# Kernel optimization log

Hardware: AMD Instinct MI355X
Metric: run time of the kernel (lower is better)

The kernel has to match this reference:

```python
import jax, jax.numpy as jnp
import numpy as np

B, D_IN, D_H, N = 16, 32, 64, 4000
ORDER = 2
C_CAT = D_IN + D_H            # 96 channels into each gate conv
C_EFF = (ORDER + 1) * C_CAT   # 288 after order-K diffusion concat


def setup_inputs() -> dict:
    key = jax.random.key(0)
    ks = jax.random.split(key, 9)
    x = jax.random.normal(ks[0], (B, D_IN, N), dtype=jnp.float32)
    h = jax.random.normal(ks[1], (B, D_H, N), dtype=jnp.float32)
    # uniform adjacency, roughly row-normalized to keep diffusion stable
    adj = jax.random.uniform(ks[2], (N, N), dtype=jnp.float32) / N
    scale = 0.05
    Wf = jax.random.normal(ks[3], (D_H, C_EFF), dtype=jnp.float32) * scale
    Wu = jax.random.normal(ks[4], (D_H, C_EFF), dtype=jnp.float32) * scale
    Wc = jax.random.normal(ks[5], (D_H, C_EFF), dtype=jnp.float32) * scale
    bf = jax.random.normal(ks[6], (D_H,), dtype=jnp.float32) * scale
    bu = jax.random.normal(ks[7], (D_H,), dtype=jnp.float32) * scale
    bc = jax.random.normal(ks[8], (D_H,), dtype=jnp.float32) * scale
    return {"x": x, "h": h, "adj": adj, "Wf": Wf, "bf": bf,
            "Wu": Wu, "bu": bu, "Wc": Wc, "bc": bc}


def _spatial_conv(z, adj, W, b):
    # z: [b, c, n]; order-2 diffusion: concat [z, A z, A^2 z] then 1x1 conv
    z1 = jnp.einsum('mn,bcn->bcm', adj, z)
    z2 = jnp.einsum('mn,bcn->bcm', adj, z1)
    feats = jnp.concatenate([z, z1, z2], axis=1)           # [b, 3c, n]
    return jnp.einsum('oc,bcn->bon', W, feats) + b[None, :, None]


def reference(x, h, adj, Wf, bf, Wu, bu, Wc, bc):
    x_gates = jnp.concatenate([x, h], axis=1)              # [b, d_in+d_h, n]
    r = jax.nn.sigmoid(_spatial_conv(x_gates, adj, Wf, bf))
    u = jax.nn.sigmoid(_spatial_conv(x_gates, adj, Wu, bu))
    x_c = jnp.concatenate([x, r * h], axis=1)
    c = jnp.tanh(_spatial_conv(x_c, adj, Wc, bc))
    return u * h + (1.0 - u) * c
```

## Files before the change

### kernel.cpp

```cpp
#include <hip/hip_runtime.h>
#include <cstdint>


#define NREAL 4000
#define NPAD  4096

typedef unsigned short u16;
typedef __attribute__((ext_vector_type(8))) short short8;
typedef __attribute__((ext_vector_type(4))) float f32x4;
typedef __attribute__((ext_vector_type(4))) unsigned short u16x4;

__device__ __forceinline__ u16 f2bf(float f) {
  unsigned u = __builtin_bit_cast(unsigned, f);
  return (u16)((u + 0x7FFFu + ((u >> 16) & 1u)) >> 16);
}
__device__ __forceinline__ float bf2f(u16 b) {
  unsigned u = ((unsigned)b) << 16;
  return __builtin_bit_cast(float, u);
}

__global__ __launch_bounds__(256) void k_pack_adj(const float* __restrict__ adj,
                                                  u16* __restrict__ out) {
  const int idx = blockIdx.x * 256 + threadIdx.x;
  const int m = idx >> 10;
  const int n0 = (idx & 1023) << 2;
  u16x4 o;
  if (m < NREAL && n0 < NREAL) {
    const float4 v = *reinterpret_cast<const float4*>(&adj[(long)m * NREAL + n0]);
    o.x = f2bf(v.x); o.y = f2bf(v.y); o.z = f2bf(v.z); o.w = f2bf(v.w);
  } else {
    o.x = 0; o.y = 0; o.z = 0; o.w = 0;
  }
  *reinterpret_cast<u16x4*>(&out[(long)m * NPAD + n0]) = o;
}

__global__ __launch_bounds__(256) void k_pack_zg(const float* __restrict__ x,
                                                 const float* __restrict__ h,
                                                 u16* __restrict__ zg) {
  const int idx = blockIdx.x * 256 + threadIdx.x;
  const int row = idx >> 10;
  const int n0 = (idx & 1023) << 2;
  const int b = row / 96, c = row % 96;
  const float* src = (c < 32) ? &x[((long)b * 32 + c) * NREAL]
                              : &h[((long)b * 64 + (c - 32)) * NREAL];
  u16x4 o;
  if (n0 < NREAL) {
    const float4 v = *reinterpret_cast<const float4*>(&src[n0]);
    o.x = f2bf(v.x); o.y = f2bf(v.y); o.z = f2bf(v.z); o.w = f2bf(v.w);
  } else {
    o.x = 0; o.y = 0; o.z = 0; o.w = 0;
  }
  *reinterpret_cast<u16x4*>(&zg[(long)row * NPAD + n0]) = o;
}

__global__ __launch_bounds__(256) void k_pack_w(const float* __restrict__ Wf,
                                                const float* __restrict__ Wu,
                                                const float* __restrict__ Wc,
                                                float* __restrict__ Wgt,
                                                float* __restrict__ Wct) {
  const int idx = blockIdx.x * 256 + threadIdx.x;
  if (idx < 288 * 128) {
    const int c = idx >> 7, o = idx & 127;
    Wgt[idx] = (o < 64) ? Wf[o * 288 + c] : Wu[(o - 64) * 288 + c];
  }
  if (idx < 288 * 64) {
    const int c = idx >> 6, o = idx & 63;
    Wct[idx] = Wc[o * 288 + c];
  }
}

template<bool F32OUT>
__global__ __launch_bounds__(256) void k_gemm_bt(const u16* __restrict__ A,
                                                 const u16* __restrict__ B,
                                                 void* __restrict__ Cout,
                                                 int ktPerChunk, long chunkElems) {
  __shared__ __align__(16) u16 As[128 * 32];
  __shared__ __align__(16) u16 Bs[128 * 32];
  const int tid = threadIdx.x;
  const int wave = tid >> 6;
  const int lane = tid & 63;
  const int bn = blockIdx.x;
  const int bm = blockIdx.y;
  const int ktBegin = blockIdx.z * ktPerChunk;
  const int ktEnd = ktBegin + ktPerChunk;

  const int srow = (wave << 4) + (lane >> 2);
  const int sslot = (lane & 3) << 3;
  const long aRow  = (long)(bm * 128 + srow) * NPAD;
  const long aRow2 = aRow + 64L * NPAD;
  const long bRow  = (long)(bn * 128 + srow) * NPAD;
  const long bRow2 = bRow + 64L * NPAD;
  const int wbase = __builtin_amdgcn_readfirstlane(wave << 9);

  const int wr = (wave >> 1) << 6;
  const int wc = (wave & 1) << 6;
  const int fr = lane & 15;
  const int ks = (lane >> 4) << 3;

  f32x4 acc[4][4] = {};

  for (int kt = ktBegin; kt < ktEnd; ++kt) {
    const long kofs = (long)kt * 32 + sslot;
    __syncthreads();
    __builtin_amdgcn_global_load_lds(
        (const __attribute__((address_space(1))) void*)(A + aRow + kofs),
        (__attribute__((address_space(3))) void*)(&As[wbase]), 16, 0, 0);
    __builtin_amdgcn_global_load_lds(
        (const __attribute__((address_space(1))) void*)(A + aRow2 + kofs),
        (__attribute__((address_space(3))) void*)(&As[wbase + 2048]), 16, 0, 0);
    __builtin_amdgcn_global_load_lds(
        (const __attribute__((address_space(1))) void*)(B + bRow + kofs),
        (__attribute__((address_space(3))) void*)(&Bs[wbase]), 16, 0, 0);
    __builtin_amdgcn_global_load_lds(
        (const __attribute__((address_space(1))) void*)(B + bRow2 + kofs),
        (__attribute__((address_space(3))) void*)(&Bs[wbase + 2048]), 16, 0, 0);
    __syncthreads();

    short8 av[4], bv[4];
#pragma unroll
    for (int i = 0; i < 4; ++i) {
      av[i] = *reinterpret_cast<const short8*>(&As[(wr + (i << 4) + fr) * 32 + ks]);
      bv[i] = *reinterpret_cast<const short8*>(&Bs[(wc + (i << 4) + fr) * 32 + ks]);
    }
#pragma unroll
    for (int i = 0; i < 4; ++i)
#pragma unroll
      for (int j = 0; j < 4; ++j)
        acc[i][j] = __builtin_amdgcn_mfma_f32_16x16x32_bf16(av[i], bv[j], acc[i][j], 0, 0, 0);
  }

  const int rb = bm * 128 + wr + ((lane >> 4) << 2);
  const int cb = bn * 128 + wc + fr;
  if (F32OUT) {
    float* C = (float*)Cout + (long)blockIdx.z * chunkElems;
#pragma unroll
    for (int i = 0; i < 4; ++i)
#pragma unroll
      for (int j = 0; j < 4; ++j)
#pragma unroll
        for (int q = 0; q < 4; ++q)
          C[(long)(rb + (i << 4) + q) * NPAD + cb + (j << 4)] = acc[i][j][q];
  } else {
    u16* C = (u16*)Cout;
#pragma unroll
    for (int i = 0; i < 4; ++i)
#pragma unroll
      for (int j = 0; j < 4; ++j)
#pragma unroll
        for (int q = 0; q < 4; ++q)
          C[(long)(rb + (i << 4) + q) * NPAD + cb + (j << 4)] = f2bf(acc[i][j][q]);
  }
}

template<int NC>
__global__ __launch_bounds__(256) void k_combine(const float* __restrict__ P,
                                                 long chunkElems,
                                                 u16* __restrict__ out) {
  const long i4 = ((long)blockIdx.x * 256 + threadIdx.x) * 4;
  f32x4 s = *reinterpret_cast<const f32x4*>(&P[i4]);
#pragma unroll
  for (int c = 1; c < NC; ++c) {
    const f32x4 v = *reinterpret_cast<const f32x4*>(&P[(long)c * chunkElems + i4]);
    s.x += v.x; s.y += v.y; s.z += v.z; s.w += v.w;
  }
  u16x4 o;
  o.x = f2bf(s.x); o.y = f2bf(s.y); o.z = f2bf(s.z); o.w = f2bf(s.w);
  *reinterpret_cast<u16x4*>(&out[i4]) = o;
}

__global__ __launch_bounds__(512) void k_gates(
    const float* __restrict__ x, const float* __restrict__ h,
    const float* __restrict__ Wgt,
    const float* __restrict__ bfv, const float* __restrict__ buv,
    const u16* __restrict__ Z1, const u16* __restrict__ Z2,
    u16* __restrict__ rh_bf, float* __restrict__ rh_f, float* __restrict__ u_f) {
  const int lane = threadIdx.x & 63;
  const int wq = __builtin_amdgcn_readfirstlane(threadIdx.x >> 6);
  const int b = blockIdx.y;
  const int n0 = blockIdx.x * 128 + (lane << 1);
  if (n0 >= NREAL) return;
  const int ob = wq << 4;
  const float* xb = x + (long)b * 32 * NREAL + n0;
  const float* hb = h + (long)b * 64 * NREAL + n0;
  const u16* z1b = Z1 + (long)b * 96 * NPAD + n0;
  const u16* z2b = Z2 + (long)b * 96 * NPAD + n0;

  float a0[16] = {}, a1[16] = {};
#pragma unroll 4
  for (int c = 0; c < 32; ++c) {
    const float2 f = *reinterpret_cast<const float2*>(&xb[(long)c * NREAL]);
#pragma unroll
    for (int oi = 0; oi < 16; ++oi) {
      const float w = Wgt[c * 128 + ob + oi];
      a0[oi] = fmaf(w, f.x, a0[oi]); a1[oi] = fmaf(w, f.y, a1[oi]);
    }
  }
#pragma unroll 4
  for (int c = 0; c < 64; ++c) {
    const float2 f = *reinterpret_cast<const float2*>(&hb[(long)c * NREAL]);
#pragma unroll
    for (int oi = 0; oi < 16; ++oi) {
      const float w = Wgt[(32 + c) * 128 + ob + oi];
      a0[oi] = fmaf(w, f.x, a0[oi]); a1[oi] = fmaf(w, f.y, a1[oi]);
    }
  }
#pragma unroll 4
  for (int c = 0; c < 96; ++c) {
    const unsigned pv = *reinterpret_cast<const unsigned*>(&z1b[(long)c * NPAD]);
    const float f0 = bf2f((u16)(pv & 0xffff)), f1 = bf2f((u16)(pv >> 16));
#pragma unroll
    for (int oi = 0; oi < 16; ++oi) {
      const float w = Wgt[(96 + c) * 128 + ob + oi];
      a0[oi] = fmaf(w, f0, a0[oi]); a1[oi] = fmaf(w, f1, a1[oi]);
    }
  }
#pragma unroll 4
  for (int c = 0; c < 96; ++c) {
    const unsigned pv = *reinterpret_cast<const unsigned*>(&z2b[(long)c * NPAD]);
    const float f0 = bf2f((u16)(pv & 0xffff)), f1 = bf2f((u16)(pv >> 16));
#pragma unroll
    for (int oi = 0; oi < 16; ++oi) {
      const float w = Wgt[(192 + c) * 128 + ob + oi];
      a0[oi] = fmaf(w, f0, a0[oi]); a1[oi] = fmaf(w, f1, a1[oi]);
    }
  }

  if (wq < 4) {
#pragma unroll
    for (int oi = 0; oi < 16; ++oi) {
      const int og = ob + oi;
      const float bb = bfv[og];
      const float r0 = 1.f / (1.f + __expf(-(a0[oi] + bb)));
      const float r1 = 1.f / (1.f + __expf(-(a1[oi] + bb)));
      const float2 hv = *reinterpret_cast<const float2*>(&hb[(long)og * NREAL]);
      const float rh0 = r0 * hv.x, rh1 = r1 * hv.y;
      if (rh_f)
        *reinterpret_cast<float2*>(&rh_f[((long)b * 64 + og) * NREAL + n0]) =
            make_float2(rh0, rh1);
      const unsigned pk = (unsigned)f2bf(rh0) | ((unsigned)f2bf(rh1) << 16);
      *reinterpret_cast<unsigned*>(&rh_bf[((long)b * 64 + og) * NPAD + n0]) = pk;
    }
  } else {
#pragma unroll
    for (int oi = 0; oi < 16; ++oi) {
      const int og = (ob - 64) + oi;
      const float bb = buv[og];
      const float u0 = 1.f / (1.f + __expf(-(a0[oi] + bb)));
      const float u1 = 1.f / (1.f + __expf(-(a1[oi] + bb)));
      *reinterpret_cast<float2*>(&u_f[((long)b * 64 + og) * NREAL + n0]) =
          make_float2(u0, u1);
    }
  }
}

template<bool RHF32>
__global__ __launch_bounds__(512) void k_cand(
    const float* __restrict__ x, const float* __restrict__ h,
    const float* __restrict__ Wct, const float* __restrict__ bcv,
    const u16* __restrict__ Z1, const u16* __restrict__ Z2,
    const u16* __restrict__ Rhb, const u16* __restrict__ Rh1,
    const u16* __restrict__ Rh2,
    const float* __restrict__ rh_f, const float* __restrict__ u_f,
    float* __restrict__ out) {
  const int lane = threadIdx.x & 63;
  const int wq = __builtin_amdgcn_readfirstlane(threadIdx.x >> 6);
  const int ob = (wq & 3) << 4;
  const int n = blockIdx.x * 128 + ((wq >> 2) << 6) + lane;
  const int b = blockIdx.y;
  if (n >= NREAL) return;
  const float* xb = x + (long)b * 32 * NREAL + n;
  const float* hb = h + (long)b * 64 * NREAL + n;
  const u16* z1b = Z1 + (long)b * 96 * NPAD + n;
  const u16* z2b = Z2 + (long)b * 96 * NPAD + n;
  const u16* r1b = Rh1 + (long)b * 64 * NPAD + n;
  const u16* r2b = Rh2 + (long)b * 64 * NPAD + n;
  const float* rfb = rh_f + (long)b * 64 * NREAL + n;
  const u16* rbb = Rhb + (long)b * 64 * NPAD + n;

  float acc[16] = {};
#pragma unroll 4
  for (int c = 0; c < 32; ++c) {
    const float f = xb[(long)c * NREAL];
#pragma unroll
    for (int oi = 0; oi < 16; ++oi)
      acc[oi] = fmaf(Wct[c * 64 + ob + oi], f, acc[oi]);
  }
#pragma unroll 4
  for (int c = 0; c < 64; ++c) {
    const float f = RHF32 ? rfb[(long)c * NREAL] : bf2f(rbb[(long)c * NPAD]);
#pragma unroll
    for (int oi = 0; oi < 16; ++oi)
      acc[oi] = fmaf(Wct[(32 + c) * 64 + ob + oi], f, acc[oi]);
  }
#pragma unroll 4
  for (int c = 0; c < 32; ++c) {
    const float f = bf2f(z1b[(long)c * NPAD]);
#pragma unroll
    for (int oi = 0; oi < 16; ++oi)
      acc[oi] = fmaf(Wct[(96 + c) * 64 + ob + oi], f, acc[oi]);
  }
#pragma unroll 4
  for (int c = 0; c < 64; ++c) {
    const float f = bf2f(r1b[(long)c * NPAD]);
#pragma unroll
    for (int oi = 0; oi < 16; ++oi)
      acc[oi] = fmaf(Wct[(128 + c) * 64 + ob + oi], f, acc[oi]);
  }
#pragma unroll 4
  for (int c = 0; c < 32; ++c) {
    const float f = bf2f(z2b[(long)c * NPAD]);
#pragma unroll
    for (int oi = 0; oi < 16; ++oi)
      acc[oi] = fmaf(Wct[(192 + c) * 64 + ob + oi], f, acc[oi]);
  }
#pragma unroll 4
  for (int c = 0; c < 64; ++c) {
    const float f = bf2f(r2b[(long)c * NPAD]);
#pragma unroll
    for (int oi = 0; oi < 16; ++oi)
      acc[oi] = fmaf(Wct[(224 + c) * 64 + ob + oi], f, acc[oi]);
  }

#pragma unroll
  for (int oi = 0; oi < 16; ++oi) {
    const int og = ob + oi;
    float v = acc[oi] + bcv[og];
    v = fminf(fmaxf(v, -15.f), 15.f);
    const float e2 = __expf(2.f * v);
    const float cv = (e2 - 1.f) / (e2 + 1.f);
    const float u = u_f[((long)b * 64 + og) * NREAL + n];
    out[((long)b * 64 + og) * NREAL + n] = u * hb[(long)og * NREAL] + (1.f - u) * cv;
  }
}

extern "C" void kernel_launch(void* const* d_in, const int* in_sizes, int n_in,
                              void* d_out, int out_size, void* d_ws, size_t ws_size,
                              hipStream_t stream) {
  const float* x   = (const float*)d_in[0];
  const float* h   = (const float*)d_in[1];
  const float* adj = (const float*)d_in[2];
  const float* Wf  = (const float*)d_in[3];
  const float* bf_ = (const float*)d_in[4];
  const float* Wu  = (const float*)d_in[5];
  const float* bu_ = (const float*)d_in[6];
  const float* Wc  = (const float*)d_in[7];
  const float* bc_ = (const float*)d_in[8];
  float* out = (float*)d_out;

  char* p = (char*)d_ws;
  auto alloc = [&](size_t bytes) { char* r = p; p += bytes; return r; };
  u16* adjb = (u16*)alloc((size_t)NPAD * NPAD * 2);
  u16* Zg   = (u16*)alloc((size_t)1536 * NPAD * 2);
  u16* Rhb  = Zg;
  u16* Z1   = (u16*)alloc((size_t)1536 * NPAD * 2);
  u16* Z2   = (u16*)alloc((size_t)1536 * NPAD * 2);
  u16* Rh1  = (u16*)alloc((size_t)1024 * NPAD * 2);
  u16* Rh2  = (u16*)alloc((size_t)1024 * NPAD * 2);
  float* uf = (float*)alloc((size_t)16 * 64 * NREAL * 4);
  float* Wgt = (float*)alloc(288 * 128 * 4);
  float* Wct = (float*)alloc(288 * 64 * 4);
  const size_t RHFB = (size_t)16 * 64 * NREAL * 4;
  const size_t PC = (size_t)1536 * NPAD * 4;
  size_t used = (size_t)(p - (char*)d_ws);
  float* rhf = nullptr;
  if (ws_size >= used + RHFB) rhf = (float*)alloc(RHFB);
  used = (size_t)(p - (char*)d_ws);
  int split = 1;
  float* P = nullptr;
  if (ws_size >= used + 4 * PC) { split = 4; P = (float*)alloc(4 * PC); }
  else if (ws_size >= used + 2 * PC) { split = 2; P = (float*)alloc(2 * PC); }

  auto gemm = [&](const u16* A, const u16* B, u16* Cb, int M) {
    const long ce = (long)M * NPAD;
    if (split == 4) {
      k_gemm_bt<true><<<dim3(32, M / 128, 4), 256, 0, stream>>>(A, B, P, 32, ce);
      k_combine<4><<<dim3(M * 4), 256, 0, stream>>>(P, ce, Cb);
    } else if (split == 2) {
      k_gemm_bt<true><<<dim3(32, M / 128, 2), 256, 0, stream>>>(A, B, P, 64, ce);
      k_combine<2><<<dim3(M * 4), 256, 0, stream>>>(P, ce, Cb);
    } else {
      k_gemm_bt<false><<<dim3(32, M / 128, 1), 256, 0, stream>>>(A, B, Cb, 128, ce);
    }
  };

  k_pack_adj<<<dim3(NPAD * (NPAD / 4) / 256), 256, 0, stream>>>(adj, adjb);
  k_pack_zg <<<dim3(1536 * (NPAD / 4) / 256), 256, 0, stream>>>(x, h, Zg);
  k_pack_w  <<<dim3(144), 256, 0, stream>>>(Wf, Wu, Wc, Wgt, Wct);
  gemm(Zg, adjb, Z1, 1536);
  gemm(Z1, adjb, Z2, 1536);
  k_gates<<<dim3(32, 16), 512, 0, stream>>>(x, h, Wgt, bf_, bu_, Z1, Z2,
                                            Rhb, rhf, uf);
  gemm(Rhb, adjb, Rh1, 1024);
  gemm(Rh1, adjb, Rh2, 1024);
  if (rhf)
    k_cand<true><<<dim3(32, 16), 512, 0, stream>>>(x, h, Wct, bc_, Z1, Z2, Rhb,
                                                   Rh1, Rh2, rhf, uf, out);
  else
    k_cand<false><<<dim3(32, 16), 512, 0, stream>>>(x, h, Wct, bc_, Z1, Z2, Rhb,
                                                    Rh1, Rh2, rhf, uf, out);
}
```

Before: 546.6 us.

## Replace GEMM with 256x256 double-buffered swizzled-LDS MFMA kernel and per-GEMM split-K

Replaces the 128x128, single-buffered, K=32 GEMM with a 512-thread 256x256 tile kernel using K=64 steps. Tiles are double-buffered in LDS and the next tile is prefetched while the current one computes, with an XOR swizzle to avoid bank conflicts and raised wave priority around the MFMAs. Split-K is now chosen per GEMM (2 for the 1536-row GEMMs, up to 4 for the 1024-row ones) to keep enough blocks in flight. The larger tiles cut global and LDS traffic per FLOP, at the cost of 128KB of LDS, more registers per thread, and fewer blocks in the grid.

```diff
diff --git a/kernel.cpp b/kernel.cpp
--- a/kernel.cpp
+++ b/kernel.cpp
@@ -70,85 +70,105 @@
 }
 
 template<bool F32OUT>
-__global__ __launch_bounds__(256) void k_gemm_bt(const u16* __restrict__ A,
-                                                 const u16* __restrict__ B,
-                                                 void* __restrict__ Cout,
-                                                 int ktPerChunk, long chunkElems) {
-  __shared__ __align__(16) u16 As[128 * 32];
-  __shared__ __align__(16) u16 Bs[128 * 32];
+__global__ __launch_bounds__(512, 2) void k_gemm256(const u16* __restrict__ A,
+                                                    const u16* __restrict__ B,
+                                                    void* __restrict__ Cout,
+                                                    int ktPerChunk, long chunkElems) {
+  __shared__ __align__(16) u16 As[2][256 * 64];
+  __shared__ __align__(16) u16 Bs[2][256 * 64];
   const int tid = threadIdx.x;
-  const int wave = tid >> 6;
   const int lane = tid & 63;
-  const int bn = blockIdx.x;
-  const int bm = blockIdx.y;
-  const int ktBegin = blockIdx.z * ktPerChunk;
-  const int ktEnd = ktBegin + ktPerChunk;
-
-  const int srow = (wave << 4) + (lane >> 2);
-  const int sslot = (lane & 3) << 3;
-  const long aRow  = (long)(bm * 128 + srow) * NPAD;
-  const long aRow2 = aRow + 64L * NPAD;
-  const long bRow  = (long)(bn * 128 + srow) * NPAD;
-  const long bRow2 = bRow + 64L * NPAD;
-  const int wbase = __builtin_amdgcn_readfirstlane(wave << 9);
-
-  const int wr = (wave >> 1) << 6;
-  const int wc = (wave & 1) << 6;
+  const int wv = tid >> 6;
+  const int wm = wv >> 2;
+  const int wn = wv & 3;
+  const int bm = blockIdx.y, bn = blockIdx.x;
+
+  const int srow = tid >> 3;
+  const int jlog = (tid & 7) ^ (srow & 7);
+  const long kt0ofs = (long)blockIdx.z * ktPerChunk * 64;
+  const u16* aS = A + (long)(bm * 256 + srow) * NPAD + kt0ofs + jlog * 8;
+  const u16* bS = B + (long)(bn * 256 + srow) * NPAD + kt0ofs + jlog * 8;
+  const int ldst = tid * 8;
+
   const int fr = lane & 15;
-  const int ks = (lane >> 4) << 3;
-
-  f32x4 acc[4][4] = {};
-
-  for (int kt = ktBegin; kt < ktEnd; ++kt) {
-    const long kofs = (long)kt * 32 + sslot;
-    __syncthreads();
-    __builtin_amdgcn_global_load_lds(
-        (const __attribute__((address_space(1))) void*)(A + aRow + kofs),
-        (__attribute__((address_space(3))) void*)(&As[wbase]), 16, 0, 0);
-    __builtin_amdgcn_global_load_lds(
-        (const __attribute__((address_space(1))) void*)(A + aRow2 + kofs),
-        (__attribute__((address_space(3))) void*)(&As[wbase + 2048]), 16, 0, 0);
-    __builtin_amdgcn_global_load_lds(
-        (const __attribute__((address_space(1))) void*)(B + bRow + kofs),
-        (__attribute__((address_space(3))) void*)(&Bs[wbase]), 16, 0, 0);
-    __builtin_amdgcn_global_load_lds(
-        (const __attribute__((address_space(1))) void*)(B + bRow2 + kofs),
-        (__attribute__((address_space(3))) void*)(&Bs[wbase + 2048]), 16, 0, 0);
-    __syncthreads();
-
-    short8 av[4], bv[4];
-#pragma unroll
-    for (int i = 0; i < 4; ++i) {
-      av[i] = *reinterpret_cast<const short8*>(&As[(wr + (i << 4) + fr) * 32 + ks]);
-      bv[i] = *reinterpret_cast<const short8*>(&Bs[(wc + (i << 4) + fr) * 32 + ks]);
-    }
-#pragma unroll
-    for (int i = 0; i < 4; ++i)
-#pragma unroll
-      for (int j = 0; j < 4; ++j)
-        acc[i][j] = __builtin_amdgcn_mfma_f32_16x16x32_bf16(av[i], bv[j], acc[i][j], 0, 0, 0);
-  }
-
-  const int rb = bm * 128 + wr + ((lane >> 4) << 2);
-  const int cb = bn * 128 + wc + fr;
+  const int ksub2 = ((lane >> 4) << 3) << 1;
+
+  f32x4 acc[8][4] = {};
+
+#define STAGE(buf, kk)                                                           \
+  {                                                                              \
+    const long ko = (long)(kk) * 64;                                             \
+    _Pragma("unroll")                                                            \
+    for (int i = 0; i < 4; ++i)                                                  \
+      __builtin_amdgcn_global_load_lds(                                          \
+          (const __attribute__((address_space(1))) void*)(aS + (long)i * 64 * NPAD + ko), \
+          (__attribute__((address_space(3))) void*)(&As[buf][i * 4096 + ldst]), 16, 0, 0); \
+    _Pragma("unroll")                                                            \
+    for (int i = 0; i < 4; ++i)                                                  \
+      __builtin_amdgcn_global_load_lds(                                          \
+          (const __attribute__((address_space(1))) void*)(bS + (long)i * 64 * NPAD + ko), \
+          (__attribute__((address_space(3))) void*)(&Bs[buf][i * 4096 + ldst]), 16, 0, 0); \
+  }
+
+  STAGE(0, 0)
+  int cur = 0;
+  for (int kk = 0; kk < ktPerChunk; ++kk) {
+    if (kk + 1 < ktPerChunk) {
+      STAGE(cur ^ 1, kk + 1)
+      asm volatile("s_waitcnt vmcnt(8)\ns_barrier" ::: "memory");
+    } else {
+      asm volatile("s_waitcnt vmcnt(0)\ns_barrier" ::: "memory");
+    }
+    const char* Ab = (const char*)&As[cur][0];
+    const char* Bb = (const char*)&Bs[cur][0];
+#pragma unroll
+    for (int ks = 0; ks < 2; ++ks) {
+      const int k2 = (ks << 6) + ksub2;
+      short8 av[8], bv[4];
+#pragma unroll
+      for (int mi = 0; mi < 8; ++mi) {
+        const int row = (wm << 7) + (mi << 4) + fr;
+        av[mi] = *(const short8*)(Ab + row * 128 + (k2 ^ ((row & 7) << 4)));
+      }
+#pragma unroll
+      for (int ni = 0; ni < 4; ++ni) {
+        const int row = (wn << 6) + (ni << 4) + fr;
+        bv[ni] = *(const short8*)(Bb + row * 128 + (k2 ^ ((row & 7) << 4)));
+      }
+      __builtin_amdgcn_s_setprio(1);
+#pragma unroll
+      for (int mi = 0; mi < 8; ++mi)
+#pragma unroll
+        for (int ni = 0; ni < 4; ++ni)
+          acc[mi][ni] = __builtin_amdgcn_mfma_f32_16x16x32_bf16(av[mi], bv[ni],
+                                                                acc[mi][ni], 0, 0, 0);
+      __builtin_amdgcn_s_setprio(0);
+    }
+    asm volatile("s_barrier" ::: "memory");
+    cur ^= 1;
+  }
+#undef STAGE
+
+  const int rb = bm * 256 + (wm << 7) + ((lane >> 4) << 2);
+  const int cb = bn * 256 + (wn << 6) + fr;
   if (F32OUT) {
     float* C = (float*)Cout + (long)blockIdx.z * chunkElems;
 #pragma unroll
-    for (int i = 0; i < 4; ++i)
-#pragma unroll
-      for (int j = 0; j < 4; ++j)
+    for (int mi = 0; mi < 8; ++mi)
+#pragma unroll
+      for (int ni = 0; ni < 4; ++ni)
 #pragma unroll
         for (int q = 0; q < 4; ++q)
-          C[(long)(rb + (i << 4) + q) * NPAD + cb + (j << 4)] = acc[i][j][q];
+          C[(long)(rb + (mi << 4) + q) * NPAD + cb + (ni << 4)] = acc[mi][ni][q];
   } else {
     u16* C = (u16*)Cout;
 #pragma unroll
-    for (int i = 0; i < 4; ++i)
-#pragma unroll
-      for (int j = 0; j < 4; ++j)
+    for (int mi = 0; mi < 8; ++mi)
+#pragma unroll
+      for (int ni = 0; ni < 4; ++ni)
 #pragma unroll
         for (int q = 0; q < 4; ++q)
-          C[(long)(rb + (i << 4) + q) * NPAD + cb + (j << 4)] = f2bf(acc[i][j][q]);
+          C[(long)(rb + (mi << 4) + q) * NPAD + cb + (ni << 4)] = f2bf(acc[mi][ni][q]);
   }
 }
 
@@ -360,38 +380,42 @@
   float* Wgt = (float*)alloc(288 * 128 * 4);
   float* Wct = (float*)alloc(288 * 64 * 4);
   const size_t RHFB = (size_t)16 * 64 * NREAL * 4;
-  const size_t PC = (size_t)1536 * NPAD * 4;
   size_t used = (size_t)(p - (char*)d_ws);
   float* rhf = nullptr;
   if (ws_size >= used + RHFB) rhf = (float*)alloc(RHFB);
   used = (size_t)(p - (char*)d_ws);
-  int split = 1;
+
+  const size_t PZ2 = (size_t)2 * 1536 * NPAD * 4;
+  const size_t PR4 = (size_t)4 * 1024 * NPAD * 4;
+  int sZ = 1, sR = 1;
   float* P = nullptr;
-  if (ws_size >= used + 4 * PC) { split = 4; P = (float*)alloc(4 * PC); }
-  else if (ws_size >= used + 2 * PC) { split = 2; P = (float*)alloc(2 * PC); }
-
-  auto gemm = [&](const u16* A, const u16* B, u16* Cb, int M) {
+  if (ws_size >= used + PR4)      { P = (float*)alloc(PR4); sZ = 2; sR = 4; }
+  else if (ws_size >= used + PZ2) { P = (float*)alloc(PZ2); sZ = 2; sR = 2; }
+
+  auto gemm = [&](const u16* Ax, const u16* Bx, u16* Cb, int M, int sk) {
     const long ce = (long)M * NPAD;
-    if (split == 4) {
-      k_gemm_bt<true><<<dim3(32, M / 128, 4), 256, 0, stream>>>(A, B, P, 32, ce);
+    const int mt = M / 256;
+    const int kpc = 64 / sk;
+    if (sk == 4) {
+      k_gemm256<true><<<dim3(16, mt, 4), 512, 0, stream>>>(Ax, Bx, P, kpc, ce);
       k_combine<4><<<dim3(M * 4), 256, 0, stream>>>(P, ce, Cb);
-    } else if (split == 2) {
-      k_gemm_bt<true><<<dim3(32, M / 128, 2), 256, 0, stream>>>(A, B, P, 64, ce);
+    } else if (sk == 2) {
+      k_gemm256<true><<<dim3(16, mt, 2), 512, 0, stream>>>(Ax, Bx, P, kpc, ce);
       k_combine<2><<<dim3(M * 4), 256, 0, stream>>>(P, ce, Cb);
     } else {
-      k_gemm_bt<false><<<dim3(32, M / 128, 1), 256, 0, stream>>>(A, B, Cb, 128, ce);
+      k_gemm256<false><<<dim3(16, mt, 1), 512, 0, stream>>>(Ax, Bx, Cb, 64, ce);
     }
   };
 
   k_pack_adj<<<dim3(NPAD * (NPAD / 4) / 256), 256, 0, stream>>>(adj, adjb);
   k_pack_zg <<<dim3(1536 * (NPAD / 4) / 256), 256, 0, stream>>>(x, h, Zg);
   k_pack_w  <<<dim3(144), 256, 0, stream>>>(Wf, Wu, Wc, Wgt, Wct);
-  gemm(Zg, adjb, Z1, 1536);
-  gemm(Z1, adjb, Z2, 1536);
+  gemm(Zg, adjb, Z1, 1536, sZ);
+  gemm(Z1, adjb, Z2, 1536, sZ);
   k_gates<<<dim3(32, 16), 512, 0, stream>>>(x, h, Wgt, bf_, bu_, Z1, Z2,
                                             Rhb, rhf, uf);
-  gemm(Rhb, adjb, Rh1, 1024);
-  gemm(Rh1, adjb, Rh2, 1024);
+  gemm(Rhb, adjb, Rh1, 1024, sR);
+  gemm(Rh1, adjb, Rh2, 1024, sR);
   if (rhf)
     k_cand<true><<<dim3(32, 16), 512, 0, stream>>>(x, h, Wct, bc_, Z1, Z2, Rhb,
                                                    Rh1, Rh2, rhf, uf, out);
```

Result: faster. 495.1 us (-9.4%).
